# Performance work log

Hardware: AMD Instinct MI355X
Metric: run time of the kernel (lower is better)

Reference implementation:

```python
import jax, jax.numpy as jnp
import numpy as np

B, S, E, H = 4, 2048, 768, 12
D = E // H  # 64

def setup_inputs() -> dict:
    key = jax.random.key(0)
    k1, k2, k3, k4, k5 = jax.random.split(key, 5)
    x = jax.random.normal(k1, (B, S, E), dtype=jnp.float32)
    att_mask = jnp.ones((B, S), dtype=jnp.int32)
    # parameters (stored transposed vs torch: [in, out])
    W_attn = jax.random.normal(k2, (E, 3 * E), dtype=jnp.float32) * (1.0 / np.sqrt(E))
    b_attn = jax.random.normal(k3, (3 * E,), dtype=jnp.float32) * 0.02
    W_proj = jax.random.normal(k4, (E, E), dtype=jnp.float32) * (1.0 / np.sqrt(E))
    b_proj = jax.random.normal(k5, (E,), dtype=jnp.float32) * 0.02
    return {"x": x, "W_attn": W_attn, "b_attn": b_attn,
            "W_proj": W_proj, "b_proj": b_proj, "att_mask": att_mask}

def reference(x, W_attn, b_attn, W_proj, b_proj, att_mask):
    b, s, e = x.shape
    qkv = x @ W_attn + b_attn                       # [B,S,3E]
    q, k, v = jnp.split(qkv, 3, axis=-1)
    # [B,H,S,D]
    q = q.reshape(b, s, H, D).transpose(0, 2, 1, 3)
    k = k.reshape(b, s, H, D).transpose(0, 2, 1, 3)
    v = v.reshape(b, s, H, D).transpose(0, 2, 1, 3)
    att = jnp.einsum('bhqd,bhkd->bhqk', q, k) * (1.0 / np.sqrt(D))
    causal = jnp.tril(jnp.ones((s, s), dtype=bool))          # [S,S]
    mask = causal[None, None] & (att_mask[:, None, None, :] != 0)  # [B,1,S,S]
    att = jnp.where(mask, att, -jnp.inf)
    att = jax.nn.softmax(att, axis=-1)
    y = jnp.einsum('bhqk,bhkd->bhqd', att, v)       # [B,H,S,D]
    y = y.transpose(0, 2, 1, 3).reshape(b, s, e)
    return y @ W_proj + b_proj
```

## Files before the change

### kernel.cpp

```cpp
#include <hip/hip_runtime.h>
#include <cstdint>


typedef __bf16 bf16x8 __attribute__((ext_vector_type(8)));
typedef __bf16 bf16x4 __attribute__((ext_vector_type(4)));
typedef float  f32x4  __attribute__((ext_vector_type(4)));
typedef float  f32x16 __attribute__((ext_vector_type(16)));

#define MFMA16(a, b, c) __builtin_amdgcn_mfma_f32_16x16x32_bf16(a, b, c, 0, 0, 0)
#define MFMA32(a, b, c) __builtin_amdgcn_mfma_f32_32x32x16_bf16(a, b, c, 0, 0, 0)

static constexpr int Bb = 4, Ss = 2048, Ee = 768, Hh = 12, Dd = 64;

__device__ __forceinline__ void gl2lds16(const void* g, void* l) {
  __builtin_amdgcn_global_load_lds(
      (const __attribute__((address_space(1))) void*)g,
      (__attribute__((address_space(3))) void*)l, 16, 0, 0);
}

__global__ void cast_f32_bf16(const float* __restrict__ x,
                              __bf16* __restrict__ y, int n) {
  int i = (blockIdx.x * blockDim.x + threadIdx.x) * 4;
  if (i < n) {
    float4 v = *(const float4*)(x + i);
    bf16x4 o = {(__bf16)v.x, (__bf16)v.y, (__bf16)v.z, (__bf16)v.w};
    *(bf16x4*)(y + i) = o;
  }
}

__global__ void transpose_cast(const float* __restrict__ W,
                               __bf16* __restrict__ Wt, int K, int N) {
  __shared__ float t[64][65];
  const int k0 = blockIdx.y * 64, n0 = blockIdx.x * 64;
#pragma unroll
  for (int i = 0; i < 16; ++i) {
    int lin = i * 256 + threadIdx.x;
    int r = lin >> 6, c = lin & 63;
    t[r][c] = W[(size_t)(k0 + r) * N + n0 + c];
  }
  __syncthreads();
#pragma unroll
  for (int i = 0; i < 16; ++i) {
    int lin = i * 256 + threadIdx.x;
    int r = lin >> 6, c = lin & 63;
    Wt[(size_t)(n0 + r) * K + k0 + c] = (__bf16)t[c][r];
  }
}

template <int MODE>
__global__ __launch_bounds__(256) void gemm_bt(
    const __bf16* __restrict__ A, const __bf16* __restrict__ Bt,
    const float* __restrict__ bias, __bf16* __restrict__ Qb,
    __bf16* __restrict__ Kb, __bf16* __restrict__ VTb,
    float* __restrict__ out, int K, int N) {
  __shared__ __align__(16) __bf16 As[128 * 32];
  __shared__ __align__(16) __bf16 Bs[128 * 32];
  const int tid = threadIdx.x;
  const int wave = tid >> 6, lane = tid & 63;
  const int quad = lane >> 4, c16 = lane & 15;
  const int m0 = blockIdx.y * 128, n0 = blockIdx.x * 128;
  const int wm = (wave >> 1) * 64, wn = (wave & 1) * 64;

  f32x4 acc[4][4] = {};

  for (int k0 = 0; k0 < K; k0 += 32) {
    __syncthreads();
#pragma unroll
    for (int i = 0; i < 2; ++i) {
      const int cb = (i * 4 + wave) * 64;
      const int c = cb + lane;
      const int row = c >> 2, kk = (c & 3) * 8;
      gl2lds16(&A[(size_t)(m0 + row) * K + k0 + kk], &As[cb * 8]);
      gl2lds16(&Bt[(size_t)(n0 + row) * K + k0 + kk], &Bs[cb * 8]);
    }
    __syncthreads();
    bf16x8 af[4], bf[4];
#pragma unroll
    for (int mi = 0; mi < 4; ++mi)
      af[mi] = *(const bf16x8*)&As[(wm + mi * 16 + c16) * 32 + quad * 8];
#pragma unroll
    for (int ni = 0; ni < 4; ++ni)
      bf[ni] = *(const bf16x8*)&Bs[(wn + ni * 16 + c16) * 32 + quad * 8];
#pragma unroll
    for (int mi = 0; mi < 4; ++mi)
#pragma unroll
      for (int ni = 0; ni < 4; ++ni)
        acc[mi][ni] = MFMA16(af[mi], bf[ni], acc[mi][ni]);
  }

#pragma unroll
  for (int mi = 0; mi < 4; ++mi) {
#pragma unroll
    for (int ni = 0; ni < 4; ++ni) {
      const int gcol = n0 + wn + ni * 16 + c16;
      const float bv = bias[gcol];
      const int growb = m0 + wm + mi * 16 + quad * 4;
      if (MODE == 0) {
        const int which = gcol / Ee;
        const int e = gcol - which * Ee;
        const int hh = e >> 6, dd = e & 63;
        const int bb = growb >> 11, ss = growb & 2047;
        const size_t bh = (size_t)(bb * Hh + hh);
        if (which == 2) {
          bf16x4 o;
#pragma unroll
          for (int r = 0; r < 4; ++r) o[r] = (__bf16)(acc[mi][ni][r] + bv);
          *(bf16x4*)&VTb[(bh * Dd + dd) * Ss + ss] = o;
        } else if (which == 0) {
#pragma unroll
          for (int r = 0; r < 4; ++r)
            Qb[(bh * Ss + ss + r) * Dd + dd] =
                (__bf16)((acc[mi][ni][r] + bv) * 0.125f);
        } else {
#pragma unroll
          for (int r = 0; r < 4; ++r)
            Kb[(bh * Ss + ss + r) * Dd + dd] = (__bf16)(acc[mi][ni][r] + bv);
        }
      } else {
#pragma unroll
        for (int r = 0; r < 4; ++r)
          out[(size_t)(growb + r) * N + gcol] = acc[mi][ni][r] + bv;
      }
    }
  }
}

__global__ __launch_bounds__(256, 3) void flash_attn(
    const __bf16* __restrict__ Qb, const __bf16* __restrict__ Kb,
    const __bf16* __restrict__ VTb, const int* __restrict__ amask,
    __bf16* __restrict__ Yb) {
  const int bid = blockIdx.x;
  const int xcd = bid & 7, j = bid >> 3;
  const int bh = xcd * 6 + (j >> 4);
  const int T = 15 - (j & 15);
  const int b = bh / Hh, h = bh - b * Hh;
  const int tid = threadIdx.x, w = tid >> 6, lane = tid & 63;
  const int hl = lane >> 5, l31 = lane & 31;
  const __bf16* Qp = Qb + (size_t)bh * Ss * Dd;
  const __bf16* Kp = Kb + (size_t)bh * Ss * Dd;
  const __bf16* Vp = VTb + (size_t)bh * Dd * Ss;

  __shared__ __align__(16) __bf16 KtP[64][72];
  __shared__ __align__(16) __bf16 VtP[64][72];

  const int qb = T * 128 + w * 32;
  const int qg = qb + l31;

  bf16x8 qf[4];
#pragma unroll
  for (int wd = 0; wd < 4; ++wd) {
    bf16x4 a0 = *(const bf16x4*)&Qp[(size_t)qg * Dd + wd * 16 + hl * 4];
    bf16x4 a1 = *(const bf16x4*)&Qp[(size_t)qg * Dd + wd * 16 + 8 + hl * 4];
    qf[wd] = bf16x8{a0[0], a0[1], a0[2], a0[3], a1[0], a1[1], a1[2], a1[3]};
  }

  f32x16 yacc[2] = {};
  float m_i = -1e4f, l_i = 0.f;

  const int nkt = 2 * T + 2;
  for (int kt = 0; kt < nkt; ++kt) {
    const int k0 = kt * 64;
    __syncthreads();
#pragma unroll
    for (int i = 0; i < 2; ++i) {
      const int c = i * 256 + tid;
      const int row = c >> 3, cc = c & 7;
      const int wd = cc >> 1, u = cc & 1;
      bf16x8 kv = *(const bf16x8*)&Kp[(size_t)(k0 + row) * Dd + cc * 8];
      *(bf16x4*)&KtP[row][wd * 16 + u * 4] = bf16x4{kv[0], kv[1], kv[2], kv[3]};
      *(bf16x4*)&KtP[row][wd * 16 + 8 + u * 4] =
          bf16x4{kv[4], kv[5], kv[6], kv[7]};
      bf16x8 vv = *(const bf16x8*)&Vp[(size_t)row * Ss + k0 + cc * 8];
      *(bf16x4*)&VtP[row][wd * 16 + u * 4] = bf16x4{vv[0], vv[1], vv[2], vv[3]};
      *(bf16x4*)&VtP[row][wd * 16 + 8 + u * 4] =
          bf16x4{vv[4], vv[5], vv[6], vv[7]};
    }
    const uint64_t mball = __ballot(amask[b * Ss + k0 + lane] != 0);
    __syncthreads();

    if (k0 > qb + 31) continue;

    f32x16 sg[2];
#pragma unroll
    for (int g = 0; g < 2; ++g) {
      f32x16 acc = {};
#pragma unroll
      for (int wd = 0; wd < 4; ++wd) {
        const bf16x8 kf =
            *(const bf16x8*)&KtP[g * 32 + l31][wd * 16 + hl * 8];
        acc = MFMA32(kf, qf[wd], acc);
      }
      sg[g] = acc;
    }

    if (k0 + 63 > qb) {
#pragma unroll
      for (int g = 0; g < 2; ++g)
#pragma unroll
        for (int r = 0; r < 16; ++r) {
          const int key = k0 + g * 32 + (r & 3) + 8 * (r >> 2) + 4 * hl;
          sg[g][r] = (key <= qg) ? sg[g][r] : -30000.f;
        }
    }
    if (mball != ~0ull) {
#pragma unroll
      for (int g = 0; g < 2; ++g)
#pragma unroll
        for (int r = 0; r < 16; ++r) {
          const int kr = g * 32 + (r & 3) + 8 * (r >> 2) + 4 * hl;
          sg[g][r] = ((mball >> kr) & 1) ? sg[g][r] : -30000.f;
        }
    }

    float mx = sg[0][0];
#pragma unroll
    for (int r = 1; r < 16; ++r) mx = fmaxf(mx, sg[0][r]);
#pragma unroll
    for (int r = 0; r < 16; ++r) mx = fmaxf(mx, sg[1][r]);
    mx = fmaxf(mx, __shfl_xor(mx, 32));
    const float mnew = fmaxf(m_i, mx);
    const float alpha = __expf(m_i - mnew);
    float rs = 0.f;
#pragma unroll
    for (int g = 0; g < 2; ++g)
#pragma unroll
      for (int r = 0; r < 16; ++r) {
        const float e = __expf(sg[g][r] - mnew);
        sg[g][r] = e;
        rs += e;
      }
    rs += __shfl_xor(rs, 32);
    l_i = l_i * alpha + rs;
    m_i = mnew;
#pragma unroll
    for (int dt = 0; dt < 2; ++dt)
#pragma unroll
      for (int r = 0; r < 16; ++r) yacc[dt][r] *= alpha;

    bf16x8 pf[4];
#pragma unroll
    for (int W = 0; W < 4; ++W) {
      bf16x8 f;
#pragma unroll
      for (int jj = 0; jj < 8; ++jj)
        f[jj] = (__bf16)sg[W >> 1][8 * (W & 1) + jj];
      pf[W] = f;
    }

#pragma unroll
    for (int dt = 0; dt < 2; ++dt)
#pragma unroll
      for (int W = 0; W < 4; ++W) {
        const bf16x8 vf =
            *(const bf16x8*)&VtP[dt * 32 + l31][W * 16 + hl * 8];
        yacc[dt] = MFMA32(vf, pf[W], yacc[dt]);
      }
  }

  const float inv = 1.f / l_i;
  __bf16* yrow = Yb + (size_t)(b * Ss + qg) * Ee + h * Dd;
#pragma unroll
  for (int dt = 0; dt < 2; ++dt)
#pragma unroll
    for (int s = 0; s < 4; ++s) {
      bf16x4 o;
#pragma unroll
      for (int r = 0; r < 4; ++r) o[r] = (__bf16)(yacc[dt][s * 4 + r] * inv);
      *(bf16x4*)&yrow[dt * 32 + s * 8 + hl * 4] = o;
    }
}

extern "C" void kernel_launch(void* const* d_in, const int* in_sizes, int n_in,
                              void* d_out, int out_size, void* d_ws,
                              size_t ws_size, hipStream_t stream) {
  const float* x      = (const float*)d_in[0];
  const float* W_attn = (const float*)d_in[1];
  const float* b_attn = (const float*)d_in[2];
  const float* W_proj = (const float*)d_in[3];
  const float* b_proj = (const float*)d_in[4];
  const int* att_mask = (const int*)d_in[5];
  float* out = (float*)d_out;

  char* ws = (char*)d_ws;
  __bf16* xb  = (__bf16*)(ws);
  __bf16* Wat = (__bf16*)(ws + 12582912);
  __bf16* Wpt = (__bf16*)(ws + 16121856);
  __bf16* Qb  = (__bf16*)(ws + 17301504);
  __bf16* Kb  = (__bf16*)(ws + 29884416);
  __bf16* VTb = (__bf16*)(ws + 42467328);
  __bf16* Yb  = xb;

  cast_f32_bf16<<<6144, 256, 0, stream>>>(x, xb, Bb * Ss * Ee);
  transpose_cast<<<dim3(36, 12), 256, 0, stream>>>(W_attn, Wat, Ee, 3 * Ee);
  transpose_cast<<<dim3(12, 12), 256, 0, stream>>>(W_proj, Wpt, Ee, Ee);

  gemm_bt<0><<<dim3(18, 64), 256, 0, stream>>>(xb, Wat, b_attn, Qb, Kb, VTb,
                                               nullptr, Ee, 3 * Ee);
  flash_attn<<<768, 256, 0, stream>>>(Qb, Kb, VTb, att_mask, Yb);
  gemm_bt<1><<<dim3(6, 64), 256, 0, stream>>>(Yb, Wpt, b_proj, nullptr,
                                              nullptr, nullptr, out, Ee, Ee);
}
```

Baseline: 237.8 us.

## Pipeline flash attention K/V loads with async LDS triple buffering and exp2

The attention kernel now stages K and V tiles straight into LDS with async global_load_lds into a triple buffer, using an XOR swizzle in place of padded rows. Waits go through explicit vmcnt-based barriers, so loads overlap with compute. The QKV GEMM epilogue stores Q/K/V with a permuted column order, so fragments load as one contiguous 16-byte read, and Q is pre-scaled by log2(e)/8 so softmax can use exp2. Work is balanced across waves by pairing short and long causal query strips within each block, and the mask ballots are computed once up front. The cost is more LDS use and tighter coupling between the GEMM store layout and the attention kernel.

After: 231.5 us. 1.03x faster.

```diff
diff --git a/kernel.cpp b/kernel.cpp
--- a/kernel.cpp
+++ b/kernel.cpp
@@ -11,11 +11,24 @@
 #define MFMA32(a, b, c) __builtin_amdgcn_mfma_f32_32x32x16_bf16(a, b, c, 0, 0, 0)
 
 static constexpr int Bb = 4, Ss = 2048, Ee = 768, Hh = 12, Dd = 64;
+#define QSCALE 0.18033688011112042f
 
 __device__ __forceinline__ void gl2lds16(const void* g, void* l) {
   __builtin_amdgcn_global_load_lds(
       (const __attribute__((address_space(1))) void*)g,
       (__attribute__((address_space(3))) void*)l, 16, 0, 0);
+}
+
+__device__ __forceinline__ float fexp2(float x) {
+#if __has_builtin(__builtin_amdgcn_exp2f)
+  return __builtin_amdgcn_exp2f(x);
+#else
+  return exp2f(x);
+#endif
+}
+
+__device__ __forceinline__ int swap23(int x) {
+  return (x & ~12) | ((x & 4) << 1) | ((x & 8) >> 1);
 }
 
 __global__ void cast_f32_bf16(const float* __restrict__ x,
@@ -102,19 +115,22 @@
         const int bb = growb >> 11, ss = growb & 2047;
         const size_t bh = (size_t)(bb * Hh + hh);
         if (which == 2) {
+          const int ssp = swap23(ss);
           bf16x4 o;
 #pragma unroll
           for (int r = 0; r < 4; ++r) o[r] = (__bf16)(acc[mi][ni][r] + bv);
-          *(bf16x4*)&VTb[(bh * Dd + dd) * Ss + ss] = o;
+          *(bf16x4*)&VTb[(bh * Dd + dd) * Ss + ssp] = o;
         } else if (which == 0) {
+          const int ddp = swap23(dd);
 #pragma unroll
           for (int r = 0; r < 4; ++r)
-            Qb[(bh * Ss + ss + r) * Dd + dd] =
-                (__bf16)((acc[mi][ni][r] + bv) * 0.125f);
+            Qb[(bh * Ss + ss + r) * Dd + ddp] =
+                (__bf16)((acc[mi][ni][r] + bv) * QSCALE);
         } else {
+          const int ddp = swap23(dd);
 #pragma unroll
           for (int r = 0; r < 4; ++r)
-            Kb[(bh * Ss + ss + r) * Dd + dd] = (__bf16)(acc[mi][ni][r] + bv);
+            Kb[(bh * Ss + ss + r) * Dd + ddp] = (__bf16)(acc[mi][ni][r] + bv);
         }
       } else {
 #pragma unroll
@@ -132,53 +148,72 @@
   const int bid = blockIdx.x;
   const int xcd = bid & 7, j = bid >> 3;
   const int bh = xcd * 6 + (j >> 4);
-  const int T = 15 - (j & 15);
+  const int bidx = j & 15;
   const int b = bh / Hh, h = bh - b * Hh;
   const int tid = threadIdx.x, w = tid >> 6, lane = tid & 63;
   const int hl = lane >> 5, l31 = lane & 31;
+  const int r7 = l31 & 7;
+
+  const int s = ((w & 2) << 4) + ((w & 1) ? 31 - bidx : bidx);
+  const int qs = s * 32;
+  const int qg = qs + l31;
+  const int ktmax = s >> 1;
+  const int nkt = ((63 - bidx) >> 1) + 1;
+
   const __bf16* Qp = Qb + (size_t)bh * Ss * Dd;
   const __bf16* Kp = Kb + (size_t)bh * Ss * Dd;
   const __bf16* Vp = VTb + (size_t)bh * Dd * Ss;
 
-  __shared__ __align__(16) __bf16 KtP[64][72];
-  __shared__ __align__(16) __bf16 VtP[64][72];
-
-  const int qb = T * 128 + w * 32;
-  const int qg = qb + l31;
+  __shared__ __align__(16) __bf16 Ksh[3 * 64 * 64];
+  __shared__ __align__(16) __bf16 Vsh[3 * 64 * 64];
+  __shared__ uint64_t ballots[32];
 
   bf16x8 qf[4];
 #pragma unroll
-  for (int wd = 0; wd < 4; ++wd) {
-    bf16x4 a0 = *(const bf16x4*)&Qp[(size_t)qg * Dd + wd * 16 + hl * 4];
-    bf16x4 a1 = *(const bf16x4*)&Qp[(size_t)qg * Dd + wd * 16 + 8 + hl * 4];
-    qf[wd] = bf16x8{a0[0], a0[1], a0[2], a0[3], a1[0], a1[1], a1[2], a1[3]};
-  }
+  for (int wd = 0; wd < 4; ++wd)
+    qf[wd] = *(const bf16x8*)&Qp[(size_t)qg * Dd + wd * 16 + hl * 8];
+
+#pragma unroll
+  for (int i = 0; i < 8; ++i) {
+    const int t = w * 8 + i;
+    const uint64_t ball = __ballot(amask[b * Ss + t * 64 + lane] != 0);
+    if (lane == 0) ballots[t] = ball;
+  }
+  asm volatile("s_waitcnt lgkmcnt(0)" ::: "memory");
+
+  auto stage = [&](int kt, int buf) {
+    __bf16* kb = &Ksh[buf * 4096];
+    __bf16* vb = &Vsh[buf * 4096];
+    const char* ksrc = (const char*)(Kp + (size_t)kt * 64 * Dd);
+    const char* vsrc = (const char*)Vp + (size_t)kt * 128;
+#pragma unroll
+    for (int i = 0; i < 2; ++i) {
+      const int cb = i * 256 + w * 64;
+      const int p = cb + lane;
+      const int row = p >> 3;
+      const int cc = (p & 7) ^ (row & 7);
+      gl2lds16(ksrc + (size_t)row * 128 + cc * 16, &kb[cb * 8]);
+      gl2lds16(vsrc + (size_t)row * 4096 + cc * 16, &vb[cb * 8]);
+    }
+  };
+
+  stage(0, 0);
+  if (nkt > 1) stage(1, 1);
 
   f32x16 yacc[2] = {};
-  float m_i = -1e4f, l_i = 0.f;
-
-  const int nkt = 2 * T + 2;
+  float m_i = -30000.f, l_i = 0.f;
+
   for (int kt = 0; kt < nkt; ++kt) {
+    if (kt + 1 < nkt)
+      asm volatile("s_waitcnt vmcnt(4)\n\ts_barrier" ::: "memory");
+    else
+      asm volatile("s_waitcnt vmcnt(0)\n\ts_barrier" ::: "memory");
+    if (kt + 2 < nkt) stage(kt + 2, (kt + 2) % 3);
+
+    if (kt > ktmax) continue;
     const int k0 = kt * 64;
-    __syncthreads();
-#pragma unroll
-    for (int i = 0; i < 2; ++i) {
-      const int c = i * 256 + tid;
-      const int row = c >> 3, cc = c & 7;
-      const int wd = cc >> 1, u = cc & 1;
-      bf16x8 kv = *(const bf16x8*)&Kp[(size_t)(k0 + row) * Dd + cc * 8];
-      *(bf16x4*)&KtP[row][wd * 16 + u * 4] = bf16x4{kv[0], kv[1], kv[2], kv[3]};
-      *(bf16x4*)&KtP[row][wd * 16 + 8 + u * 4] =
-          bf16x4{kv[4], kv[5], kv[6], kv[7]};
-      bf16x8 vv = *(const bf16x8*)&Vp[(size_t)row * Ss + k0 + cc * 8];
-      *(bf16x4*)&VtP[row][wd * 16 + u * 4] = bf16x4{vv[0], vv[1], vv[2], vv[3]};
-      *(bf16x4*)&VtP[row][wd * 16 + 8 + u * 4] =
-          bf16x4{vv[4], vv[5], vv[6], vv[7]};
-    }
-    const uint64_t mball = __ballot(amask[b * Ss + k0 + lane] != 0);
-    __syncthreads();
-
-    if (k0 > qb + 31) continue;
+    const __bf16* kb = &Ksh[(kt % 3) * 4096];
+    const __bf16* vb = &Vsh[(kt % 3) * 4096];
 
     f32x16 sg[2];
 #pragma unroll
@@ -186,14 +221,14 @@
       f32x16 acc = {};
 #pragma unroll
       for (int wd = 0; wd < 4; ++wd) {
-        const bf16x8 kf =
-            *(const bf16x8*)&KtP[g * 32 + l31][wd * 16 + hl * 8];
+        const bf16x8 kf = *(const bf16x8*)&kb[(g * 32 + l31) * 64 +
+                                             (((2 * wd + hl) ^ r7) * 8)];
         acc = MFMA32(kf, qf[wd], acc);
       }
       sg[g] = acc;
     }
 
-    if (k0 + 63 > qb) {
+    if (k0 + 63 > qs) {
 #pragma unroll
       for (int g = 0; g < 2; ++g)
 #pragma unroll
@@ -202,6 +237,7 @@
           sg[g][r] = (key <= qg) ? sg[g][r] : -30000.f;
         }
     }
+    const uint64_t mball = ballots[kt];
     if (mball != ~0ull) {
 #pragma unroll
       for (int g = 0; g < 2; ++g)
@@ -219,13 +255,13 @@
     for (int r = 0; r < 16; ++r) mx = fmaxf(mx, sg[1][r]);
     mx = fmaxf(mx, __shfl_xor(mx, 32));
     const float mnew = fmaxf(m_i, mx);
-    const float alpha = __expf(m_i - mnew);
+    const float alpha = fexp2(m_i - mnew);
     float rs = 0.f;
 #pragma unroll
     for (int g = 0; g < 2; ++g)
 #pragma unroll
       for (int r = 0; r < 16; ++r) {
-        const float e = __expf(sg[g][r] - mnew);
+        const float e = fexp2(sg[g][r] - mnew);
         sg[g][r] = e;
         rs += e;
       }
@@ -251,8 +287,8 @@
     for (int dt = 0; dt < 2; ++dt)
 #pragma unroll
       for (int W = 0; W < 4; ++W) {
-        const bf16x8 vf =
-            *(const bf16x8*)&VtP[dt * 32 + l31][W * 16 + hl * 8];
+        const bf16x8 vf = *(const bf16x8*)&vb[(dt * 32 + l31) * 64 +
+                                             (((2 * W + hl) ^ r7) * 8)];
         yacc[dt] = MFMA32(vf, pf[W], yacc[dt]);
       }
   }
@@ -262,11 +298,12 @@
 #pragma unroll
   for (int dt = 0; dt < 2; ++dt)
 #pragma unroll
-    for (int s = 0; s < 4; ++s) {
+    for (int sreg = 0; sreg < 4; ++sreg) {
       bf16x4 o;
 #pragma unroll
-      for (int r = 0; r < 4; ++r) o[r] = (__bf16)(yacc[dt][s * 4 + r] * inv);
-      *(bf16x4*)&yrow[dt * 32 + s * 8 + hl * 4] = o;
+      for (int r = 0; r < 4; ++r)
+        o[r] = (__bf16)(yacc[dt][sreg * 4 + r] * inv);
+      *(bf16x4*)&yrow[dt * 32 + sreg * 8 + hl * 4] = o;
     }
 }
 
```
